# Optimization experiments

Hardware: AMD Instinct MI355X
Metric: run time of the kernel (lower is better)

The kernel has to match this reference:

```python
import jax, jax.numpy as jnp
import numpy as np

N = 50000   # nodes
E = 400000  # edges
D = 128     # hidden = out dim
H = 4       # heads
DH = 32     # head dim (D // H)
T = 3       # node types
R = 6       # relation (edge) types
L = 2       # layers
EPS = 1e-5


def setup_inputs() -> dict:
    key = jax.random.key(0)
    ks = jax.random.split(key, 12)
    s = D ** -0.5
    sh = DH ** -0.5
    return {
        "h": jax.random.normal(ks[0], (N, D), jnp.float32),
        "src": jax.random.randint(ks[1], (E,), 0, N),
        "dst": jax.random.randint(ks[2], (E,), 0, N),
        "ntype": jnp.sort(jax.random.randint(ks[3], (N,), 0, T)),
        "etype": jnp.sort(jax.random.randint(ks[4], (E,), 0, R)),
        # per-layer HGTConv params (stacked over L)
        "Wk": jax.random.normal(ks[5], (L, T, D, D), jnp.float32) * s,
        "Wq": jax.random.normal(ks[6], (L, T, D, D), jnp.float32) * s,
        "Wv": jax.random.normal(ks[7], (L, T, D, D), jnp.float32) * s,
        "Wa": jax.random.normal(ks[8], (L, T, D, D), jnp.float32) * s,
        "W_att": jax.random.normal(ks[9], (L, H, R, DH, DH), jnp.float32) * sh,
        "W_msg": jax.random.normal(ks[10], (L, H, R, DH, DH), jnp.float32) * sh,
        "pri": jnp.ones((L, H, R), jnp.float32),
        "skip": jnp.ones((L, T), jnp.float32),
        "ln_g": jnp.ones((L, D), jnp.float32),
        "ln_b": jnp.zeros((L, D), jnp.float32),
        # LayerAggregator params
        "agg_w": jnp.ones((L,), jnp.float32),
        "agg_g": jnp.ones((D,), jnp.float32),
        "agg_b": jnp.zeros((D,), jnp.float32),
    }


def typed_linear(x, types, W):
    # W: [T, in, out]; per-node-type linear (DGL TypedLinear, no bias)
    out = x @ W[0]
    for t in range(1, W.shape[0]):
        out = jnp.where((types == t)[:, None], x @ W[t], out)
    return out


def edge_typed(x, etype, W):
    # x: [E, H, DH]; W: [H, R, DH, DH]; per-relation, per-head linear
    out = jnp.einsum('ehd,hdo->eho', x, W[:, 0])
    for r in range(1, W.shape[1]):
        out = jnp.where((etype == r)[:, None, None],
                        jnp.einsum('ehd,hdo->eho', x, W[:, r]), out)
    return out


def layer_norm(x, g, b):
    mu = x.mean(-1, keepdims=True)
    var = ((x - mu) ** 2).mean(-1, keepdims=True)
    return (x - mu) * jax.lax.rsqrt(var + EPS) * g + b


def hgt_layer(x, src, dst, ntype, etype, Wk, Wq, Wv, Wa, W_att, W_msg, pri, skip):
    n = x.shape[0]
    k = typed_linear(x, ntype, Wk).reshape(n, H, DH)
    q = typed_linear(x, ntype, Wq).reshape(n, H, DH)
    v = typed_linear(x, ntype, Wv).reshape(n, H, DH)
    kw = edge_typed(k[src], etype, W_att)          # [E,H,DH]
    mv = edge_typed(v[src], etype, W_msg)          # [E,H,DH]
    a = (kw * q[dst]).sum(-1) * pri.T[etype] / np.sqrt(DH).astype(np.float32)  # [E,H]
    # edge softmax over destination nodes
    mx = jax.lax.stop_gradient(jax.ops.segment_max(a, dst, num_segments=n))
    ex = jnp.exp(a - mx[dst])
    den = jax.ops.segment_sum(ex, dst, num_segments=n)
    att = ex / den[dst]                             # [E,H]
    agg = jax.ops.segment_sum(att[:, :, None] * mv, dst, num_segments=n)
    h_a = typed_linear(agg.reshape(n, H * DH), ntype, Wa)
    sk = jax.nn.sigmoid(skip)[ntype][:, None]
    return h_a * sk + x * (1.0 - sk)                # skip gate (dropout = eval identity)


def reference(h, src, dst, ntype, etype, Wk, Wq, Wv, Wa, W_att, W_msg,
              pri, skip, ln_g, ln_b, agg_w, agg_g, agg_b):
    x = h
    outs = []
    for l in range(L):
        ho = hgt_layer(x, src, dst, ntype, etype, Wk[l], Wq[l], Wv[l], Wa[l],
                       W_att[l], W_msg[l], pri[l], skip[l])
        # residual is Identity (in_dim == out_dim), dropout is eval-mode identity
        x = layer_norm(x + ho, ln_g[l], ln_b[l])
        outs.append(x)
    w = jax.nn.softmax(agg_w)
    mixed = sum(w[i] * outs[i] for i in range(L))
    return layer_norm(mixed, agg_g, agg_b)  # [N, D]; per-type dict is just slicing by ntype
```

## Files before the change

### kernel.cpp

```cpp
#include <hip/hip_runtime.h>

#define NN 50000
#define NE 400000
#define DD 128
#define HH 4
#define DHH 32
#define TT 3
#define RR 6
#define LL 2
#define EPSF 1e-5f

typedef unsigned short ushort_t;
typedef unsigned int uint_t;
typedef __attribute__((ext_vector_type(8))) short short8_t;
typedef __attribute__((ext_vector_type(4))) float float4_t;
typedef __attribute__((ext_vector_type(4))) uint_t uint4v;

__device__ inline ushort_t f2bf(float f){
  union { float f; uint_t u; } x; x.f = f;
  uint_t r = x.u + 0x7fffu + ((x.u >> 16) & 1u);
  return (ushort_t)(r >> 16);
}
__device__ inline float bf2f(ushort_t u){
  union { uint_t u; float f; } x; x.u = ((uint_t)u) << 16;
  return x.f;
}
__device__ inline uint_t pack2(float a, float b){
  return (uint_t)f2bf(a) | ((uint_t)f2bf(b) << 16);
}

__global__ void hist_kernel(const int* __restrict__ dst, int* __restrict__ cnt){
  int e = blockIdx.x*256 + threadIdx.x;
  if (e < NE) atomicAdd(&cnt[dst[e]], 1);
}

__global__ void scan_kernel(const int* __restrict__ deg, int* __restrict__ rowptr){
  __shared__ int wsum[16];
  __shared__ int carrySh;
  int tid = threadIdx.x, lane = tid & 63, w = tid >> 6;
  if (tid == 0){ carrySh = 0; rowptr[0] = 0; }
  __syncthreads();
  for (int base = 0; base < NN; base += 1024){
    int i = base + tid;
    int v = (i < NN) ? deg[i] : 0;
    int s = v;
    #pragma unroll
    for (int off=1; off<64; off<<=1){ int t = __shfl_up(s, off); if (lane >= off) s += t; }
    if (lane == 63) wsum[w] = s;
    __syncthreads();
    if (w == 0 && lane < 16){
      int t = wsum[lane];
      #pragma unroll
      for (int off=1; off<16; off<<=1){ int u = __shfl_up(t, off); if (lane >= off) t += u; }
      wsum[lane] = t;
    }
    __syncthreads();
    int waveOff = (w == 0) ? 0 : wsum[w-1];
    int incl = s + waveOff + carrySh;
    if (i < NN) rowptr[i+1] = incl;
    __syncthreads();
    if (tid == 0) carrySh += wsum[15];
    __syncthreads();
  }
}

__global__ void scatter_kernel(const int* __restrict__ dst, const int* __restrict__ src,
                               const int* __restrict__ etype, const int* __restrict__ rowptr,
                               int* __restrict__ cnt, uint_t* __restrict__ sr, int* __restrict__ dp){
  int e = blockIdx.x*256 + threadIdx.x;
  if (e < NE){
    int d = dst[e];
    int pos = rowptr[d] + atomicAdd(&cnt[d], 1);
    sr[pos] = (uint_t)src[e] | ((uint_t)etype[e] << 27);
    dp[pos] = d;
  }
}

__global__ void wprep_kernel(const float* __restrict__ Wk, const float* __restrict__ Wq,
                             const float* __restrict__ Wv, const float* __restrict__ Wa,
                             ushort_t* __restrict__ Wkf, ushort_t* __restrict__ Wqf,
                             ushort_t* __restrict__ Wvf, ushort_t* __restrict__ Waf){
  int i = blockIdx.x*256 + threadIdx.x;
  if (i < TT*DD*DD){
    int j = i & 7, m = (i>>3)&15, kg = (i>>7)&3, ks = (i>>9)&3, tile = (i>>11)&7, t = i>>14;
    int d = ks*32 + kg*4 + (j&3) + ((j>>2)<<4);
    int o = tile*16 + m;
    size_t srcI = (size_t)t*16384 + (size_t)d*DD + o;
    Wkf[i] = f2bf(Wk[srcI]);
    Wqf[i] = f2bf(Wq[srcI]);
    Wvf[i] = f2bf(Wv[srcI]);
    Waf[i] = f2bf(Wa[srcI]);
  }
}

__global__ void wprep2_kernel(const float* __restrict__ Watt, const float* __restrict__ Wmsg,
                              ushort_t* __restrict__ Wattf, ushort_t* __restrict__ Wmsgf){
  int i = blockIdx.x*256 + threadIdx.x;
  if (i < HH*RR*DHH*DHH){
    int j = i & 7, m = (i>>3)&15, kg = (i>>7)&3;
    int tile = (i>>9) % 12, h = i / 6144;
    int nout = tile*16 + m;
    int r = nout >> 5, dd = nout & 31;
    int k = kg*4 + (j&3) + ((j>>2)<<4);
    Wattf[i] = f2bf(Watt[(((h*RR + r)*DHH + dd)<<5) + k]);
    Wmsgf[i] = f2bf(Wmsg[(((h*RR + r)*DHH + k)<<5) + dd]);
  }
}

__global__ __launch_bounds__(256) void kqv_kernel(
    const float* __restrict__ x, const int* __restrict__ ntype,
    const float* __restrict__ Wk, const float* __restrict__ Wq, const float* __restrict__ Wv,
    const ushort_t* __restrict__ Wkf, const ushort_t* __restrict__ Wqf, const ushort_t* __restrict__ Wvf,
    const ushort_t* __restrict__ Wattf, const ushort_t* __restrict__ Wmsgf,
    const float* __restrict__ pri,
    ushort_t* __restrict__ kout, ushort_t* __restrict__ qh, ushort_t* __restrict__ vhat)
{
  __shared__ int nts[16];
  __shared__ ushort_t smem[24704];
  ushort_t* xs_ = smem;
  ushort_t* qs_ = smem + 2112;
  ushort_t* vs_ = smem + 4224;
  ushort_t* ks_ = smem + 6336;
  ushort_t* stg1 = smem;
  ushort_t* stg2 = smem + 12352;
  int tid = threadIdx.x;
  int n0 = blockIdx.x * 16;
  if (tid < 16) nts[tid] = ntype[n0 + tid];
  #pragma unroll
  for (int it=0; it<8; it++){
    int i = tid + it*256;
    xs_[(i>>7)*132 + (i&127)] = f2bf(x[(size_t)n0*DD + i]);
  }
  __syncthreads();
  int t0 = nts[0];
  bool uni = true;
  #pragma unroll
  for (int j=1;j<16;j++) uni = uni && (nts[j] == t0);

  int lane = tid & 63;
  union U8 { struct { uint2 lo, hi; } u; short8_t s; uint4 q; };

  if (uni){
    int w = tid >> 6;
    int m = lane & 15, kg = lane >> 4;
    float4_t acck0{0.f,0.f,0.f,0.f}, acck1{0.f,0.f,0.f,0.f};
    float4_t accq0{0.f,0.f,0.f,0.f}, accq1{0.f,0.f,0.f,0.f};
    float4_t accv0{0.f,0.f,0.f,0.f}, accv1{0.f,0.f,0.f,0.f};
    const ushort_t* wkf = Wkf + (size_t)t0*16384;
    const ushort_t* wqf = Wqf + (size_t)t0*16384;
    const ushort_t* wvf = Wvf + (size_t)t0*16384;
    int tA = 2*w, tB = 2*w+1;
    #pragma unroll
    for (int ks=0; ks<4; ks++){
      U8 a_;
      a_.u.lo = *(const uint2*)&xs_[m*132 + ks*32 + kg*4];
      a_.u.hi = *(const uint2*)&xs_[m*132 + ks*32 + kg*4 + 16];
      int offA = (((tA*4 + ks)*4 + kg) << 7) + (m << 3);
      int offB = (((tB*4 + ks)*4 + kg) << 7) + (m << 3);
      U8 bk0, bk1, bq0, bq1, bv0, bv1;
      bk0.q = *(const uint4*)(wkf + offA);
      bk1.q = *(const uint4*)(wkf + offB);
      bq0.q = *(const uint4*)(wqf + offA);
      bq1.q = *(const uint4*)(wqf + offB);
      bv0.q = *(const uint4*)(wvf + offA);
      bv1.q = *(const uint4*)(wvf + offB);
      acck0 = __builtin_amdgcn_mfma_f32_16x16x32_bf16(bk0.s, a_.s, acck0, 0,0,0);
      acck1 = __builtin_amdgcn_mfma_f32_16x16x32_bf16(bk1.s, a_.s, acck1, 0,0,0);
      accq0 = __builtin_amdgcn_mfma_f32_16x16x32_bf16(bq0.s, a_.s, accq0, 0,0,0);
      accq1 = __builtin_amdgcn_mfma_f32_16x16x32_bf16(bq1.s, a_.s, accq1, 0,0,0);
      accv0 = __builtin_amdgcn_mfma_f32_16x16x32_bf16(bv0.s, a_.s, accv0, 0,0,0);
      accv1 = __builtin_amdgcn_mfma_f32_16x16x32_bf16(bv1.s, a_.s, accv1, 0,0,0);
    }
    int cA = tA*16 + (kg<<2), cB = tB*16 + (kg<<2);
    *(uint2*)(&ks_[m*132 + cA]) = make_uint2(pack2(acck0[0],acck0[1]), pack2(acck0[2],acck0[3]));
    *(uint2*)(&ks_[m*132 + cB]) = make_uint2(pack2(acck1[0],acck1[1]), pack2(acck1[2],acck1[3]));
    *(uint2*)(&qs_[m*132 + cA]) = make_uint2(pack2(accq0[0],accq0[1]), pack2(accq0[2],accq0[3]));
    *(uint2*)(&qs_[m*132 + cB]) = make_uint2(pack2(accq1[0],accq1[1]), pack2(accq1[2],accq1[3]));
    *(uint2*)(&vs_[m*132 + cA]) = make_uint2(pack2(accv0[0],accv0[1]), pack2(accv0[2],accv0[3]));
    *(uint2*)(&vs_[m*132 + cB]) = make_uint2(pack2(accv1[0],accv1[1]), pack2(accv1[2],accv1[3]));
  } else {
    int c = tid & 127, nb = (tid >> 7) * 8;
    float ak[8], aq[8], av[8];
    #pragma unroll
    for (int j=0;j<8;j++){ ak[j]=0.f; aq[j]=0.f; av[j]=0.f; }
    #pragma unroll
    for (int j=0;j<8;j++){
      int t = nts[nb+j];
      const float* wk = Wk + (size_t)t*DD*DD + c;
      const float* wq = Wq + (size_t)t*DD*DD + c;
      const float* wv = Wv + (size_t)t*DD*DD + c;
      float sk=0.f, sq=0.f, sv=0.f;
      for (int d=0; d<DD; d++){
        float xv = bf2f(xs_[(nb+j)*132 + d]);
        sk += xv*wk[d*DD];
        sq += xv*wq[d*DD];
        sv += xv*wv[d*DD];
      }
      ak[j]=sk; aq[j]=sq; av[j]=sv;
    }
    #pragma unroll
    for (int j=0;j<8;j++){
      ks_[(nb+j)*132 + c]=f2bf(ak[j]);
      qs_[(nb+j)*132 + c]=f2bf(aq[j]);
      vs_[(nb+j)*132 + c]=f2bf(av[j]);
    }
  }
  __syncthreads();

  int h = tid >> 6;
  int m = lane & 15, kg = lane >> 4;
  U8 aq_, av_;
  aq_.u.lo = *(const uint2*)&qs_[m*132 + (h<<5) + (kg<<2)];
  aq_.u.hi = *(const uint2*)&qs_[m*132 + (h<<5) + (kg<<2) + 16];
  av_.u.lo = *(const uint2*)&vs_[m*132 + (h<<5) + (kg<<2)];
  av_.u.hi = *(const uint2*)&vs_[m*132 + (h<<5) + (kg<<2) + 16];
  {
    int row = tid >> 4, coff = (tid & 15) * 8;
    uint4v kv4;
    kv4.x = *(const uint_t*)&ks_[row*132 + coff];
    kv4.y = *(const uint_t*)&ks_[row*132 + coff + 2];
    kv4.z = *(const uint_t*)&ks_[row*132 + coff + 4];
    kv4.w = *(const uint_t*)&ks_[row*132 + coff + 6];
    __builtin_nontemporal_store(kv4, (uint4v*)(kout + (size_t)(n0+row)*DD + coff));
  }
  __syncthreads();

  const ushort_t* wqb = Wattf + h*(RR*DHH*DHH);
  const ushort_t* wvb = Wmsgf + h*(RR*DHH*DHH);

  #pragma unroll
  for (int nt=0; nt<12; nt++){
    int frag = ((nt*4 + kg)<<7) + (m<<3);
    U8 bq_;
    bq_.q = *(const uint4*)(wqb + frag);
    float4_t accq{0.f,0.f,0.f,0.f};
    accq = __builtin_amdgcn_mfma_f32_16x16x32_bf16(bq_.s, aq_.s, accq, 0,0,0);
    int nout0 = nt*16 + (kg<<2);
    int r = nout0 >> 5, dd0 = nout0 & 31;
    float scale = pri[h*RR + r] * 0.17677669529663687f;
    *(uint2*)(&stg1[m*772 + r*DD + (h<<5) + dd0]) =
        make_uint2(pack2(accq[0]*scale, accq[1]*scale), pack2(accq[2]*scale, accq[3]*scale));
  }
  __syncthreads();

  #pragma unroll
  for (int it=0; it<6; it++){
    int idx = tid + it*256;
    int row = idx / 96;
    int off = (idx - row*96) * 8;
    uint4v q4;
    q4.x = *(const uint_t*)&stg1[row*772 + off];
    q4.y = *(const uint_t*)&stg1[row*772 + off + 2];
    q4.z = *(const uint_t*)&stg1[row*772 + off + 4];
    q4.w = *(const uint_t*)&stg1[row*772 + off + 6];
    __builtin_nontemporal_store(q4, (uint4v*)(qh + (size_t)(n0+row)*768 + off));
  }
  #pragma unroll
  for (int nt=0; nt<12; nt++){
    int frag = ((nt*4 + kg)<<7) + (m<<3);
    U8 bv_;
    bv_.q = *(const uint4*)(wvb + frag);
    float4_t accv{0.f,0.f,0.f,0.f};
    accv = __builtin_amdgcn_mfma_f32_16x16x32_bf16(bv_.s, av_.s, accv, 0,0,0);
    int nout0 = nt*16 + (kg<<2);
    int r = nout0 >> 5, dd0 = nout0 & 31;
    *(uint2*)(&stg2[m*772 + r*DD + (h<<5) + dd0]) =
        make_uint2(pack2(accv[0],accv[1]), pack2(accv[2],accv[3]));
  }
  __syncthreads();

  #pragma unroll
  for (int it=0; it<6; it++){
    int idx = tid + it*256;
    int row = idx / 96;
    int off = (idx - row*96) * 8;
    uint4v v4;
    v4.x = *(const uint_t*)&stg2[row*772 + off];
    v4.y = *(const uint_t*)&stg2[row*772 + off + 2];
    v4.z = *(const uint_t*)&stg2[row*772 + off + 4];
    v4.w = *(const uint_t*)&stg2[row*772 + off + 6];
    __builtin_nontemporal_store(v4, (uint4v*)(vhat + (size_t)(n0+row)*768 + off));
  }
}

__global__ __launch_bounds__(256) void logit_kernel(
    const ushort_t* __restrict__ kb, const ushort_t* __restrict__ qh,
    const uint_t* __restrict__ src_r, const int* __restrict__ dstp,
    float* __restrict__ aout)
{
  int idx = blockIdx.x*256 + threadIdx.x;
  int p = idx >> 2;
  if (p >= NE) return;
  int h = idx & 3;
  uint_t sr = src_r[p];
  int s = (int)(sr & 0x07FFFFFFu);
  int r = (int)(sr >> 27);
  int dn = dstp[p];
  const uint_t* kr = (const uint_t*)(kb + (size_t)s*DD + (h<<5));
  const uint_t* qr = (const uint_t*)(qh + ((size_t)dn*RR + r)*DD + (h<<5));
  float a = 0.f;
  #pragma unroll
  for (int i4=0; i4<4; i4++){
    uint4 kw = ((const uint4*)kr)[i4];
    uint4 qw = ((const uint4*)qr)[i4];
    a += bf2f((ushort_t)(kw.x&0xffffu))*bf2f((ushort_t)(qw.x&0xffffu))
       + bf2f((ushort_t)(kw.x>>16))   *bf2f((ushort_t)(qw.x>>16))
       + bf2f((ushort_t)(kw.y&0xffffu))*bf2f((ushort_t)(qw.y&0xffffu))
       + bf2f((ushort_t)(kw.y>>16))   *bf2f((ushort_t)(qw.y>>16))
       + bf2f((ushort_t)(kw.z&0xffffu))*bf2f((ushort_t)(qw.z&0xffffu))
       + bf2f((ushort_t)(kw.z>>16))   *bf2f((ushort_t)(qw.z>>16))
       + bf2f((ushort_t)(kw.w&0xffffu))*bf2f((ushort_t)(qw.w&0xffffu))
       + bf2f((ushort_t)(kw.w>>16))   *bf2f((ushort_t)(qw.w>>16));
  }
  aout[(size_t)p*HH + h] = a;
}

__global__ __launch_bounds__(256) void reduce_kernel(
    const ushort_t* __restrict__ vhat, const float* __restrict__ aout,
    const int* __restrict__ rowptr, const uint_t* __restrict__ src_r,
    ushort_t* __restrict__ agg16)
{
  int n = blockIdx.x*4 + (threadIdx.x >> 6);
  if (n >= NN) return;
  int lane = threadIdx.x & 63;
  int h = lane >> 4;
  int b = rowptr[n], e1 = rowptr[n+1];
  float m = -1e30f;
  for (int i=b;i<e1;i++) m = fmaxf(m, aout[(size_t)i*HH + h]);
  float den = 0.f, ac0 = 0.f, ac1 = 0.f;
  for (int i=b; i<e1; i+=8){
    int m8 = e1 - i; if (m8 > 8) m8 = 8;
    uint_t sr8[8]; float a8[8];
    #pragma unroll
    for (int jj=0;jj<8;jj++){
      int idx2 = i + ((jj < m8) ? jj : (m8-1));
      sr8[jj] = src_r[idx2];
      a8[jj] = (jj < m8) ? aout[(size_t)idx2*HH + h] : -1e30f;
    }
    uint_t vv8[8];
    #pragma unroll
    for (int jj=0;jj<8;jj++){
      uint_t sr_ = sr8[jj];
      vv8[jj] = *(const uint_t*)(vhat + ((size_t)(sr_ & 0x07FFFFFFu)*RR + (sr_>>27))*DD + (lane<<1));
    }
    #pragma unroll
    for (int jj=0;jj<8;jj++){
      float ex = __expf(a8[jj] - m);
      den += ex;
      ac0 += ex * bf2f((ushort_t)(vv8[jj] & 0xffffu));
      ac1 += ex * bf2f((ushort_t)(vv8[jj] >> 16));
    }
  }
  float inv = (den > 0.f) ? 1.f/den : 0.f;
  uint_t packed = (uint_t)f2bf(ac0*inv) | ((uint_t)f2bf(ac1*inv) << 16);
  *(uint_t*)(agg16 + (size_t)n*DD + (lane<<1)) = packed;
}

__global__ __launch_bounds__(256) void ha_kernel(
    const ushort_t* __restrict__ agg16, const float* __restrict__ x, const int* __restrict__ ntype,
    const float* __restrict__ Wa, const ushort_t* __restrict__ Waf, const float* __restrict__ skipl,
    const float* __restrict__ lng, const float* __restrict__ lnb,
    float* __restrict__ xout)
{
  __shared__ ushort_t as[16][132];
  __shared__ float xs[16][132];
  __shared__ int nts[16];
  int tid = threadIdx.x;
  int n0 = blockIdx.x * 16;
  {
    int row = tid >> 4, col = (tid & 15) * 8;
    uint4 t4 = *(const uint4*)(agg16 + (size_t)(n0+row)*DD + col);
    *(uint2*)&as[row][col]   = make_uint2(t4.x, t4.y);
    *(uint2*)&as[row][col+4] = make_uint2(t4.z, t4.w);
  }
  if (tid < 16) nts[tid] = ntype[n0 + tid];
  __syncthreads();
  int t0 = nts[0];
  bool uni = true;
  #pragma unroll
  for (int j=1;j<16;j++) uni = uni && (nts[j] == t0);

  if (uni){
    int lane = tid & 63, w = tid >> 6;
    int m = lane & 15, kg = lane >> 4;
    float4_t acc0{0.f,0.f,0.f,0.f}, acc1{0.f,0.f,0.f,0.f};
    const ushort_t* waf = Waf + (size_t)t0*16384;
    int tA = 2*w, tB = 2*w+1;
    union U8 { struct { uint2 lo, hi; } u; short8_t s; uint4 q; };
    #pragma unroll
    for (int ks=0; ks<4; ks++){
      U8 a_;
      a_.u.lo = *(const uint2*)&as[m][ks*32 + kg*4];
      a_.u.hi = *(const uint2*)&as[m][ks*32 + kg*4 + 16];
      U8 b0, b1;
      b0.q = *(const uint4*)(waf + ((((tA*4 + ks)*4 + kg) << 7) + (m << 3)));
      b1.q = *(const uint4*)(waf + ((((tB*4 + ks)*4 + kg) << 7) + (m << 3)));
      acc0 = __builtin_amdgcn_mfma_f32_16x16x32_bf16(b0.s, a_.s, acc0, 0,0,0);
      acc1 = __builtin_amdgcn_mfma_f32_16x16x32_bf16(b1.s, a_.s, acc1, 0,0,0);
    }
    float sk = 1.f/(1.f + __expf(-skipl[t0]));
    int cA = tA*16 + (kg<<2), cB = tB*16 + (kg<<2);
    #pragma unroll
    for (int i=0;i<4;i++){
      float xva = x[(size_t)(n0+m)*DD + cA + i];
      float xvb = x[(size_t)(n0+m)*DD + cB + i];
      xs[m][cA+i] = acc0[i]*sk + xva*(2.f - sk);
      xs[m][cB+i] = acc1[i]*sk + xvb*(2.f - sk);
    }
  } else {
    int c = tid & 127, nb = (tid >> 7) * 8;
    float acc[8];
    #pragma unroll
    for (int j=0;j<8;j++) acc[j]=0.f;
    #pragma unroll
    for (int j=0;j<8;j++){
      int t = nts[nb+j];
      const float* wa = Wa + (size_t)t*DD*DD + c;
      float sacc2 = 0.f;
      for (int d=0; d<DD; d++)
        sacc2 += bf2f(as[nb+j][d]) * wa[d*DD];
      acc[j] = sacc2;
    }
    #pragma unroll
    for (int j=0;j<8;j++){
      int n = n0 + nb + j;
      float sk2 = 1.f/(1.f + __expf(-skipl[nts[nb+j]]));
      float xv = x[(size_t)n*DD + c];
      xs[nb+j][c] = acc[j]*sk2 + xv*(2.f - sk2);
    }
  }
  __syncthreads();
  int lane = tid & 63;
  int r0 = tid >> 6;
  #pragma unroll
  for (int rr = r0; rr < 16; rr += 4){
    float t0v = xs[rr][lane], t1v = xs[rr][lane+64];
    float s = t0v + t1v;
    #pragma unroll
    for (int off=32; off>0; off>>=1) s += __shfl_xor(s, off);
    float mu = s * (1.f/DD);
    float d0 = t0v-mu, d1 = t1v-mu;
    float vs = d0*d0 + d1*d1;
    #pragma unroll
    for (int off=32; off>0; off>>=1) vs += __shfl_xor(vs, off);
    float inv = rsqrtf(vs*(1.f/DD) + EPSF);
    size_t base = (size_t)(n0+rr)*DD;
    xout[base+lane]    = d0*inv*lng[lane]    + lnb[lane];
    xout[base+lane+64] = d1*inv*lng[lane+64] + lnb[lane+64];
  }
}

__global__ __launch_bounds__(256) void final_kernel(
    const float* __restrict__ x1, const float* __restrict__ x2,
    const float* __restrict__ aggw, const float* __restrict__ g, const float* __restrict__ b,
    float* __restrict__ out)
{
  int lane = threadIdx.x & 63;
  int n = blockIdx.x*4 + (threadIdx.x >> 6);
  float a0 = aggw[0], a1 = aggw[1];
  float m = fmaxf(a0, a1);
  float e0 = __expf(a0-m), e1 = __expf(a1-m);
  float inv01 = 1.f/(e0+e1);
  float w0 = e0*inv01, w1 = e1*inv01;
  size_t base = (size_t)n*DD;
  float t0 = w0*x1[base+lane]    + w1*x2[base+lane];
  float t1 = w0*x1[base+lane+64] + w1*x2[base+lane+64];
  float s = t0 + t1;
  #pragma unroll
  for (int off=32; off>0; off>>=1) s += __shfl_xor(s, off);
  float mu = s * (1.f/DD);
  float d0 = t0-mu, d1 = t1-mu;
  float vs = d0*d0 + d1*d1;
  #pragma unroll
  for (int off=32; off>0; off>>=1) vs += __shfl_xor(vs, off);
  float invv = rsqrtf(vs*(1.f/DD) + EPSF);
  out[base+lane]    = d0*invv*g[lane]    + b[lane];
  out[base+lane+64] = d1*invv*g[lane+64] + b[lane+64];
}

extern "C" void kernel_launch(void* const* d_in, const int* in_sizes, int n_in,
                              void* d_out, int out_size, void* d_ws, size_t ws_size,
                              hipStream_t stream)
{
  (void)in_sizes; (void)n_in; (void)out_size; (void)ws_size;
  const float* h_in  = (const float*)d_in[0];
  const int*   src   = (const int*)d_in[1];
  const int*   dst   = (const int*)d_in[2];
  const int*   ntype = (const int*)d_in[3];
  const int*   etype = (const int*)d_in[4];
  const float* Wk    = (const float*)d_in[5];
  const float* Wq    = (const float*)d_in[6];
  const float* Wv    = (const float*)d_in[7];
  const float* Wa    = (const float*)d_in[8];
  const float* Watt  = (const float*)d_in[9];
  const float* Wmsg  = (const float*)d_in[10];
  const float* pri   = (const float*)d_in[11];
  const float* skp   = (const float*)d_in[12];
  const float* lng   = (const float*)d_in[13];
  const float* lnb   = (const float*)d_in[14];
  const float* aggw  = (const float*)d_in[15];
  const float* aggg  = (const float*)d_in[16];
  const float* aggb_ = (const float*)d_in[17];

  size_t P = (size_t)NN*DD;
  ushort_t* kb16 = (ushort_t*)d_ws;
  ushort_t* qh   = kb16 + P;
  ushort_t* vhat = qh + (size_t)NN*RR*DD;
  float* aoutb = (float*)(vhat + (size_t)NN*RR*DD);
  float* out0  = aoutb + (size_t)NE*HH;
  int* rowptr = (int*)(out0 + P);
  int* cnt    = rowptr + NN + 1;
  uint_t* srcr = (uint_t*)(cnt + NN);
  int* dstp   = (int*)(srcr + NE);
  ushort_t* wkF = (ushort_t*)(dstp + NE);
  ushort_t* wqF = wkF + (size_t)TT*DD*DD;
  ushort_t* wvF = wqF + (size_t)TT*DD*DD;
  ushort_t* waF = wvF + (size_t)TT*DD*DD;
  ushort_t* wattF = waF + (size_t)TT*DD*DD;
  ushort_t* wmsgF = wattF + (size_t)HH*RR*DHH*DHH;
  ushort_t* agg16 = qh;
  float* xout = (float*)d_out;

  hipMemsetAsync(cnt, 0, NN*sizeof(int), stream);
  hist_kernel<<<(NE+255)/256, 256, 0, stream>>>(dst, cnt);
  scan_kernel<<<1, 1024, 0, stream>>>(cnt, rowptr);
  hipMemsetAsync(cnt, 0, NN*sizeof(int), stream);
  scatter_kernel<<<(NE+255)/256, 256, 0, stream>>>(dst, src, etype, rowptr, cnt, srcr, dstp);

  const float* x = h_in;
  for (int l=0; l<LL; l++){
    const float* Wk_l  = Wk  + (size_t)l*TT*DD*DD;
    const float* Wq_l  = Wq  + (size_t)l*TT*DD*DD;
    const float* Wv_l  = Wv  + (size_t)l*TT*DD*DD;
    const float* Wa_l  = Wa  + (size_t)l*TT*DD*DD;
    const float* Wat_l = Watt + (size_t)l*HH*RR*DHH*DHH;
    const float* Wms_l = Wmsg + (size_t)l*HH*RR*DHH*DHH;
    const float* pri_l = pri + (size_t)l*HH*RR;
    const float* skp_l = skp + (size_t)l*TT;

    wprep_kernel<<<(TT*DD*DD+255)/256, 256, 0, stream>>>(Wk_l, Wq_l, Wv_l, Wa_l,
                                                         wkF, wqF, wvF, waF);
    wprep2_kernel<<<(HH*RR*DHH*DHH+255)/256, 256, 0, stream>>>(Wat_l, Wms_l, wattF, wmsgF);
    kqv_kernel<<<NN/16, 256, 0, stream>>>(x, ntype, Wk_l, Wq_l, Wv_l, wkF, wqF, wvF,
                                          wattF, wmsgF, pri_l, kb16, qh, vhat);
    logit_kernel<<<(NE*HH+255)/256, 256, 0, stream>>>(kb16, qh, srcr, dstp, aoutb);
    reduce_kernel<<<(NN+3)/4, 256, 0, stream>>>(vhat, aoutb, rowptr, srcr, agg16);
    float* xo = (l == 0) ? out0 : xout;
    ha_kernel<<<NN/16, 256, 0, stream>>>(agg16, x, ntype, Wa_l, waF, skp_l,
                                         lng + (size_t)l*DD, lnb + (size_t)l*DD, xo);
    x = xo;
  }
  final_kernel<<<NN/4, 256, 0, stream>>>(out0, xout, aggw, aggg, aggb_, xout);
}
```

Baseline: 473.0 us.

## Fuse attention logits into reduce kernel with online softmax

Removes the separate logit kernel and its E×H logit buffer. The reduce kernel now loads each destination's six per-relation query rows once into registers, gathers source K alongside V, computes dot products with a 16-lane shuffle reduction, and runs an online (rescaling) softmax. The dst-per-edge array is dropped, and nontemporal stores in kqv are replaced with plain stores so the Q/K/V outputs may stay cached for the fused consumer. The trade is extra shuffles, exp rescales and a K gather per edge inside reduce.

Result: faster. 433.2 us (-8.4%).

```diff
diff --git a/kernel.cpp b/kernel.cpp
--- a/kernel.cpp
+++ b/kernel.cpp
@@ -14,7 +14,6 @@
 typedef unsigned int uint_t;
 typedef __attribute__((ext_vector_type(8))) short short8_t;
 typedef __attribute__((ext_vector_type(4))) float float4_t;
-typedef __attribute__((ext_vector_type(4))) uint_t uint4v;
 
 __device__ inline ushort_t f2bf(float f){
   union { float f; uint_t u; } x; x.f = f;
@@ -66,13 +65,12 @@
 
 __global__ void scatter_kernel(const int* __restrict__ dst, const int* __restrict__ src,
                                const int* __restrict__ etype, const int* __restrict__ rowptr,
-                               int* __restrict__ cnt, uint_t* __restrict__ sr, int* __restrict__ dp){
+                               int* __restrict__ cnt, uint_t* __restrict__ sr){
   int e = blockIdx.x*256 + threadIdx.x;
   if (e < NE){
     int d = dst[e];
     int pos = rowptr[d] + atomicAdd(&cnt[d], 1);
     sr[pos] = (uint_t)src[e] | ((uint_t)etype[e] << 27);
-    dp[pos] = d;
   }
 }
 
@@ -216,12 +214,12 @@
   av_.u.hi = *(const uint2*)&vs_[m*132 + (h<<5) + (kg<<2) + 16];
   {
     int row = tid >> 4, coff = (tid & 15) * 8;
-    uint4v kv4;
+    uint4 kv4;
     kv4.x = *(const uint_t*)&ks_[row*132 + coff];
     kv4.y = *(const uint_t*)&ks_[row*132 + coff + 2];
     kv4.z = *(const uint_t*)&ks_[row*132 + coff + 4];
     kv4.w = *(const uint_t*)&ks_[row*132 + coff + 6];
-    __builtin_nontemporal_store(kv4, (uint4v*)(kout + (size_t)(n0+row)*DD + coff));
+    *(uint4*)(kout + (size_t)(n0+row)*DD + coff) = kv4;
   }
   __syncthreads();
 
@@ -248,12 +246,12 @@
     int idx = tid + it*256;
     int row = idx / 96;
     int off = (idx - row*96) * 8;
-    uint4v q4;
+    uint4 q4;
     q4.x = *(const uint_t*)&stg1[row*772 + off];
     q4.y = *(const uint_t*)&stg1[row*772 + off + 2];
     q4.z = *(const uint_t*)&stg1[row*772 + off + 4];
     q4.w = *(const uint_t*)&stg1[row*772 + off + 6];
-    __builtin_nontemporal_store(q4, (uint4v*)(qh + (size_t)(n0+row)*768 + off));
+    *(uint4*)(qh + (size_t)(n0+row)*768 + off) = q4;
   }
   #pragma unroll
   for (int nt=0; nt<12; nt++){
@@ -274,78 +272,69 @@
     int idx = tid + it*256;
     int row = idx / 96;
     int off = (idx - row*96) * 8;
-    uint4v v4;
+    uint4 v4;
     v4.x = *(const uint_t*)&stg2[row*772 + off];
     v4.y = *(const uint_t*)&stg2[row*772 + off + 2];
     v4.z = *(const uint_t*)&stg2[row*772 + off + 4];
     v4.w = *(const uint_t*)&stg2[row*772 + off + 6];
-    __builtin_nontemporal_store(v4, (uint4v*)(vhat + (size_t)(n0+row)*768 + off));
-  }
-}
-
-__global__ __launch_bounds__(256) void logit_kernel(
+    *(uint4*)(vhat + (size_t)(n0+row)*768 + off) = v4;
+  }
+}
+
+__global__ __launch_bounds__(256) void reduce_kernel(
     const ushort_t* __restrict__ kb, const ushort_t* __restrict__ qh,
-    const uint_t* __restrict__ src_r, const int* __restrict__ dstp,
-    float* __restrict__ aout)
-{
-  int idx = blockIdx.x*256 + threadIdx.x;
-  int p = idx >> 2;
-  if (p >= NE) return;
-  int h = idx & 3;
-  uint_t sr = src_r[p];
-  int s = (int)(sr & 0x07FFFFFFu);
-  int r = (int)(sr >> 27);
-  int dn = dstp[p];
-  const uint_t* kr = (const uint_t*)(kb + (size_t)s*DD + (h<<5));
-  const uint_t* qr = (const uint_t*)(qh + ((size_t)dn*RR + r)*DD + (h<<5));
-  float a = 0.f;
-  #pragma unroll
-  for (int i4=0; i4<4; i4++){
-    uint4 kw = ((const uint4*)kr)[i4];
-    uint4 qw = ((const uint4*)qr)[i4];
-    a += bf2f((ushort_t)(kw.x&0xffffu))*bf2f((ushort_t)(qw.x&0xffffu))
-       + bf2f((ushort_t)(kw.x>>16))   *bf2f((ushort_t)(qw.x>>16))
-       + bf2f((ushort_t)(kw.y&0xffffu))*bf2f((ushort_t)(qw.y&0xffffu))
-       + bf2f((ushort_t)(kw.y>>16))   *bf2f((ushort_t)(qw.y>>16))
-       + bf2f((ushort_t)(kw.z&0xffffu))*bf2f((ushort_t)(qw.z&0xffffu))
-       + bf2f((ushort_t)(kw.z>>16))   *bf2f((ushort_t)(qw.z>>16))
-       + bf2f((ushort_t)(kw.w&0xffffu))*bf2f((ushort_t)(qw.w&0xffffu))
-       + bf2f((ushort_t)(kw.w>>16))   *bf2f((ushort_t)(qw.w>>16));
-  }
-  aout[(size_t)p*HH + h] = a;
-}
-
-__global__ __launch_bounds__(256) void reduce_kernel(
-    const ushort_t* __restrict__ vhat, const float* __restrict__ aout,
+    const ushort_t* __restrict__ vhat,
     const int* __restrict__ rowptr, const uint_t* __restrict__ src_r,
     ushort_t* __restrict__ agg16)
 {
   int n = blockIdx.x*4 + (threadIdx.x >> 6);
   if (n >= NN) return;
   int lane = threadIdx.x & 63;
-  int h = lane >> 4;
   int b = rowptr[n], e1 = rowptr[n+1];
-  float m = -1e30f;
-  for (int i=b;i<e1;i++) m = fmaxf(m, aout[(size_t)i*HH + h]);
-  float den = 0.f, ac0 = 0.f, ac1 = 0.f;
+  const uint_t* qbase = (const uint_t*)(qh + (size_t)n*RR*DD) + lane;
+  uint_t qn0 = qbase[0*64], qn1 = qbase[1*64], qn2 = qbase[2*64];
+  uint_t qn3 = qbase[3*64], qn4 = qbase[4*64], qn5 = qbase[5*64];
+  float m = -1e30f, den = 0.f, ac0 = 0.f, ac1 = 0.f;
   for (int i=b; i<e1; i+=8){
     int m8 = e1 - i; if (m8 > 8) m8 = 8;
-    uint_t sr8[8]; float a8[8];
-    #pragma unroll
-    for (int jj=0;jj<8;jj++){
-      int idx2 = i + ((jj < m8) ? jj : (m8-1));
-      sr8[jj] = src_r[idx2];
-      a8[jj] = (jj < m8) ? aout[(size_t)idx2*HH + h] : -1e30f;
-    }
-    uint_t vv8[8];
+    uint_t sr8[8];
+    #pragma unroll
+    for (int jj=0;jj<8;jj++) sr8[jj] = src_r[i + ((jj < m8) ? jj : (m8-1))];
+    uint_t kk8[8], vv8[8];
     #pragma unroll
     for (int jj=0;jj<8;jj++){
       uint_t sr_ = sr8[jj];
-      vv8[jj] = *(const uint_t*)(vhat + ((size_t)(sr_ & 0x07FFFFFFu)*RR + (sr_>>27))*DD + (lane<<1));
-    }
+      size_t s = (size_t)(sr_ & 0x07FFFFFFu);
+      kk8[jj] = *(const uint_t*)(kb + s*DD + (lane<<1));
+      vv8[jj] = *(const uint_t*)(vhat + (s*RR + (sr_>>27))*DD + (lane<<1));
+    }
+    float p8[8];
     #pragma unroll
     for (int jj=0;jj<8;jj++){
-      float ex = __expf(a8[jj] - m);
+      int r = (int)(sr8[jj] >> 27);
+      uint_t qw = qn0;
+      qw = (r==1) ? qn1 : qw;
+      qw = (r==2) ? qn2 : qw;
+      qw = (r==3) ? qn3 : qw;
+      qw = (r==4) ? qn4 : qw;
+      qw = (r==5) ? qn5 : qw;
+      uint_t kw = kk8[jj];
+      float pp = bf2f((ushort_t)(kw & 0xffffu))*bf2f((ushort_t)(qw & 0xffffu))
+               + bf2f((ushort_t)(kw >> 16))   *bf2f((ushort_t)(qw >> 16));
+      #pragma unroll
+      for (int off=1; off<16; off<<=1) pp += __shfl_xor(pp, off);
+      p8[jj] = (jj < m8) ? pp : -1e30f;
+    }
+    float mb = p8[0];
+    #pragma unroll
+    for (int jj=1;jj<8;jj++) mb = fmaxf(mb, p8[jj]);
+    float mnew = fmaxf(m, mb);
+    float corr = __expf(m - mnew);
+    den *= corr; ac0 *= corr; ac1 *= corr;
+    m = mnew;
+    #pragma unroll
+    for (int jj=0;jj<8;jj++){
+      float ex = __expf(p8[jj] - m);
       den += ex;
       ac0 += ex * bf2f((ushort_t)(vv8[jj] & 0xffffu));
       ac1 += ex * bf2f((ushort_t)(vv8[jj] >> 16));
@@ -506,13 +495,11 @@
   ushort_t* kb16 = (ushort_t*)d_ws;
   ushort_t* qh   = kb16 + P;
   ushort_t* vhat = qh + (size_t)NN*RR*DD;
-  float* aoutb = (float*)(vhat + (size_t)NN*RR*DD);
-  float* out0  = aoutb + (size_t)NE*HH;
+  float* out0  = (float*)(vhat + (size_t)NN*RR*DD);
   int* rowptr = (int*)(out0 + P);
   int* cnt    = rowptr + NN + 1;
   uint_t* srcr = (uint_t*)(cnt + NN);
-  int* dstp   = (int*)(srcr + NE);
-  ushort_t* wkF = (ushort_t*)(dstp + NE);
+  ushort_t* wkF = (ushort_t*)(srcr + NE);
   ushort_t* wqF = wkF + (size_t)TT*DD*DD;
   ushort_t* wvF = wqF + (size_t)TT*DD*DD;
   ushort_t* waF = wvF + (size_t)TT*DD*DD;
@@ -525,7 +512,7 @@
   hist_kernel<<<(NE+255)/256, 256, 0, stream>>>(dst, cnt);
   scan_kernel<<<1, 1024, 0, stream>>>(cnt, rowptr);
   hipMemsetAsync(cnt, 0, NN*sizeof(int), stream);
-  scatter_kernel<<<(NE+255)/256, 256, 0, stream>>>(dst, src, etype, rowptr, cnt, srcr, dstp);
+  scatter_kernel<<<(NE+255)/256, 256, 0, stream>>>(dst, src, etype, rowptr, cnt, srcr);
 
   const float* x = h_in;
   for (int l=0; l<LL; l++){
@@ -543,8 +530,7 @@
     wprep2_kernel<<<(HH*RR*DHH*DHH+255)/256, 256, 0, stream>>>(Wat_l, Wms_l, wattF, wmsgF);
     kqv_kernel<<<NN/16, 256, 0, stream>>>(x, ntype, Wk_l, Wq_l, Wv_l, wkF, wqF, wvF,
                                           wattF, wmsgF, pri_l, kb16, qh, vhat);
-    logit_kernel<<<(NE*HH+255)/256, 256, 0, stream>>>(kb16, qh, srcr, dstp, aoutb);
-    reduce_kernel<<<(NN+3)/4, 256, 0, stream>>>(vhat, aoutb, rowptr, srcr, agg16);
+    reduce_kernel<<<(NN+3)/4, 256, 0, stream>>>(kb16, qh, vhat, rowptr, srcr, agg16);
     float* xo = (l == 0) ? out0 : xout;
     ha_kernel<<<NN/16, 256, 0, stream>>>(agg16, x, ntype, Wa_l, waF, skp_l,
                                          lng + (size_t)l*DD, lnb + (size_t)l*DD, xo);
```
